# Optimization experiments

Measured on AMD Instinct MI355X. Metric: run time of the kernel, lower is better.

The kernel has to match this reference:

```python
import jax, jax.numpy as jnp
import numpy as np

B, M, D, OUT = 16384, 4096, 512, 128


def setup_inputs() -> dict:
    key = jax.random.key(0)
    ks = jax.random.split(key, 5)
    x = jax.random.normal(ks[0], (B, D), dtype=jnp.float32)
    support = jax.random.normal(ks[1], (M, D), dtype=jnp.float32)
    gamma = jnp.float32(1.0)
    head_w = jax.random.normal(ks[2], (OUT, M), dtype=jnp.float32) / np.sqrt(M)
    head_b = jax.random.normal(ks[3], (OUT,), dtype=jnp.float32) * 0.01
    scale = jnp.ones((1,), dtype=jnp.float32)
    shift = jnp.zeros((1,), dtype=jnp.float32)
    return {"x": x, "support": support, "gamma": gamma,
            "head_w": head_w, "head_b": head_b,
            "scale": scale, "shift": shift}


def reference(x, support, gamma, head_w, head_b, scale, shift):
    x2 = jnp.sum(x * x, axis=-1, keepdims=True)           # [B, 1]
    s2 = jnp.sum(support * support, axis=-1)              # [M]
    xs = jnp.einsum('bd,md->bm', x, support)              # [B, M]
    sqdist = jnp.maximum(x2 + s2[None, :] - 2.0 * xs, 0.0)
    k = jnp.exp(-gamma * sqdist)                          # RBF kernel [B, M]
    out = jnp.einsum('bm,om->bo', k, head_w) + head_b     # linear head [B, OUT]
    return scale * out + shift
```

## Files before the change

kernel.cpp:

```cpp
#include <hip/hip_runtime.h>

typedef unsigned int u32;
typedef unsigned short u16;
typedef unsigned char u8;
typedef __attribute__((ext_vector_type(8))) __bf16 bf16x8;
typedef __attribute__((ext_vector_type(4))) float f32x4;

#define NB 16384
#define NM 4096
#define ND 512
#define NOUT 128
#define L2E 1.44269504088896340736f


#define WAITLG(N) do { asm volatile("s_waitcnt vmcnt(" #N ") lgkmcnt(0)" ::: "memory"); \
                       __builtin_amdgcn_sched_barrier(0); } while (0)
#define SB0() __builtin_amdgcn_sched_barrier(0)

__device__ __forceinline__ u16 f2bf(float f) {
  u32 u = __float_as_uint(f);
  u += 0x7FFFu + ((u >> 16) & 1u);
  return (u16)(u >> 16);
}

__device__ __forceinline__ u8 f2fp8(float f) {
  u32 u = __float_as_uint(f);
  u32 s = (u >> 24) & 0x80u;
  u32 au = u & 0x7FFFFFFFu;
  if (au < 0x3C800000u) return (u8)s;
  au += 0x000FFFFFu + ((au >> 20) & 1u);
  u32 e = (au >> 23) - 120u;
  u32 m = (au >> 20) & 7u;
  return (u8)(s | (e << 3) | m);
}

__device__ __forceinline__ void stage16(const void* g, void* l) {
  __builtin_amdgcn_global_load_lds((__attribute__((address_space(1))) void*)g,
                                   (__attribute__((address_space(3))) void*)l,
                                   16, 0, 0);
}

__device__ __forceinline__ uint4 pack8bf(float4 v0, float4 v1) {
  uint4 pk;
  pk.x = (u32)f2bf(v0.x) | ((u32)f2bf(v0.y) << 16);
  pk.y = (u32)f2bf(v0.z) | ((u32)f2bf(v0.w) << 16);
  pk.z = (u32)f2bf(v1.x) | ((u32)f2bf(v1.y) << 16);
  pk.w = (u32)f2bf(v1.z) | ((u32)f2bf(v1.w) << 16);
  return pk;
}

__device__ __forceinline__ uint2 pack8f8(float4 v0, float4 v1) {
  uint2 pk;
  pk.x = (u32)f2fp8(v0.x) | ((u32)f2fp8(v0.y) << 8) |
         ((u32)f2fp8(v0.z) << 16) | ((u32)f2fp8(v0.w) << 24);
  pk.y = (u32)f2fp8(v1.x) | ((u32)f2fp8(v1.y) << 8) |
         ((u32)f2fp8(v1.z) << 16) | ((u32)f2fp8(v1.w) << 24);
  return pk;
}

__global__ __launch_bounds__(256) void prep_all(const float* __restrict__ x,
                                                const float* __restrict__ s,
                                                const float* __restrict__ hw,
                                                const float* __restrict__ gamma_p,
                                                u8*  __restrict__ x_ws,
                                                u8*  __restrict__ s_ws,
                                                u16* __restrict__ hw_ws,
                                                float* __restrict__ x2g,
                                                float* __restrict__ s2g,
                                                float* __restrict__ out) {
  __shared__ uint2 t8[2048];
  __shared__ uint4 t16[2048];
  const int tid = threadIdx.x, bid = blockIdx.x;
  const int lane = tid & 63, w = tid >> 6;

  if (bid < 640) {
    const bool isx = bid < 512;
    const int blk = isx ? bid : (bid - 512);
    const float* src_m = isx ? x : s;
    u8*    dst_ws = isx ? x_ws : s_ws;
    float* sq_out = isx ? x2g : s2g;
    const float gl   = gamma_p[0] * L2E;
    const float cmul = isx ? 1.0f : (-2.0f * gl);
    const int big  = isx ? (blk >> 1) : (blk >> 2);
    const int roff = isx ? ((blk & 1) * 32) : ((blk & 3) * 32);
    const int rows = isx ? 64 : 128;

    #pragma unroll
    for (int p = 0; p < 8; ++p) {
      const int row = p * 4 + w;
      const float* src = src_m + (size_t)(blk * 32 + row) * ND + lane * 8;
      float4 v0 = *(const float4*)src;
      float4 v1 = *(const float4*)(src + 4);
      float ss = v0.x*v0.x + v0.y*v0.y + v0.z*v0.z + v0.w*v0.w
               + v1.x*v1.x + v1.y*v1.y + v1.z*v1.z + v1.w*v1.w;
      #pragma unroll
      for (int off = 32; off > 0; off >>= 1) ss += __shfl_down(ss, off);
      if (lane == 0) sq_out[blk * 32 + row] = gl * ss;
      v0.x *= cmul; v0.y *= cmul; v0.z *= cmul; v0.w *= cmul;
      v1.x *= cmul; v1.y *= cmul; v1.z *= cmul; v1.w *= cmul;
      t8[lane * 32 + ((row + lane) & 31)] = pack8f8(v0, v1);
    }
    __syncthreads();
    #pragma unroll
    for (int p = 0; p < 8; ++p) {
      const int kg = p * 8 + (tid >> 5);
      const int row = tid & 31;
      uint2 pk = t8[kg * 32 + ((row + kg) & 31)];
      *(uint2*)&dst_ws[(((size_t)(big * 64 + kg)) * rows + roff + row) * 8] = pk;
    }
  } else if (bid < 672) {
    const int blk = bid - 640;
    #pragma unroll
    for (int p = 0; p < 8; ++p) {
      const int o = p * 16 + (tid >> 4);
      const int kg = tid & 15;
      const float* src = hw + (size_t)o * NM + blk * 128 + kg * 8;
      float4 v0 = *(const float4*)src;
      float4 v1 = *(const float4*)(src + 4);
      t16[o * 16 + ((kg + o) & 15)] = pack8bf(v0, v1);
    }
    __syncthreads();
    #pragma unroll
    for (int it = 0; it < 8; ++it) {
      const int kg = it * 2 + (tid >> 7);
      const int o = tid & 127;
      uint4 pk = t16[o * 16 + ((kg + o) & 15)];
      *(uint4*)&hw_ws[(((size_t)(blk * 16 + kg)) * 128 + o) * 8] = pk;
    }
  } else {
    float4* o4 = (float4*)out;
    const float4 z = {0.f, 0.f, 0.f, 0.f};
    size_t base = (size_t)(bid - 672) * 8192 + tid;
    #pragma unroll 8
    for (int i = 0; i < 32; ++i) o4[base + (size_t)i * 256] = z;
  }
}

__global__ __launch_bounds__(256, 2)
void rbf_fused(const u8* __restrict__ x_ws, const u8* __restrict__ s_ws,
               const u16* __restrict__ hw_ws, const float* __restrict__ x2g,
               const float* __restrict__ s2g, const float* __restrict__ head_b,
               const float* __restrict__ scale_p, const float* __restrict__ shift_p,
               float* __restrict__ out)
{
  extern __shared__ __align__(16) char smem[];

  const int tid  = threadIdx.x;
  const int w    = tid >> 6;
  const int lane = tid & 63;
  const int quad = lane >> 4;
  const int l16  = lane & 15;
  const int wr   = w & 1;
  const int wc   = w >> 1;
  const int xcd  = blockIdx.x & 7;
  const int rb   = (blockIdx.x >> 3) * 2 + (xcd & 1);
  const int half = xcd >> 1;
  const int b0   = rb * 64;

  const float vscale = scale_p[0];
  const float vshift = shift_p[0];

  const u8* xsrc = x_ws + (size_t)rb * 32768;
  const u8* ssrc = s_ws + (size_t)(half * 8) * 65536;

  auto stage_grp = [&](int mt_s, int grp_s) {
    const u8* sp = ssrc + (size_t)mt_s * 65536 + grp_s * 8192;
    char* dp = smem + 32768 + (grp_s & 3) * 8192;
    stage16(sp + tid * 16, dp + tid * 16);
    stage16(sp + 4096 + tid * 16, dp + 4096 + tid * 16);
  };

  #pragma unroll
  for (int i = 0; i < 8; ++i)
    stage16(xsrc + i * 4096 + tid * 16, smem + i * 4096 + tid * 16);
  SB0();

  f32x4 x2v[2];
  #pragma unroll
  for (int r = 0; r < 2; ++r)
    x2v[r] = *(const f32x4*)&x2g[b0 + wr * 32 + r * 16 + quad * 4];

  stage_grp(0, 0); SB0();
  stage_grp(0, 1); SB0();
  stage_grp(0, 2);
  asm volatile("s_waitcnt vmcnt(4)" ::: "memory");
  SB0();
  __builtin_amdgcn_s_barrier();
  SB0();

  const f32x4 zf = {0.f, 0.f, 0.f, 0.f};
  f32x4 acc_xs[2][4];
  f32x4 acc_out[2][4];
  #pragma unroll
  for (int r = 0; r < 2; ++r)
    #pragma unroll
    for (int c = 0; c < 4; ++c) { acc_xs[r][c] = zf; acc_out[r][c] = zf; }

  bf16x8 b2a[4], b2b[4];

  #pragma unroll 1
  for (int mt = 0; mt < 8; ++mt) {
    const int mtg = half * 8 + mt;
    float s2v[4];

    #pragma unroll
    for (int grp = 0; grp < 8; ++grp) {
      if (grp == 0) {
        #pragma unroll
        for (int c = 0; c < 4; ++c)
          s2v[c] = s2g[mtg * 128 + wc * 64 + c * 16 + l16];
      }

      long long a[2][2], b[2][4];
      #pragma unroll
      for (int k2 = 0; k2 < 2; ++k2) {
        const int kc = grp * 2 + k2;
        #pragma unroll
        for (int r = 0; r < 2; ++r)
          a[k2][r] = *(const long long*)(smem + ((kc * 4 + quad) * 64 + wr * 32 + r * 16 + l16) * 8);
        #pragma unroll
        for (int c = 0; c < 4; ++c)
          b[k2][c] = *(const long long*)(smem + 32768 + (grp & 3) * 8192 +
                                         ((k2 * 4 + quad) * 128 + wc * 64 + c * 16 + l16) * 8);
      }

      bf16x8 a2[2];
      if (mt > 0 && (grp & 1) == 0) {
        const int kg = (grp >> 1) * 4 + quad;
        #pragma unroll
        for (int r = 0; r < 2; ++r)
          a2[r] = *(const bf16x8*)(smem + 65536 + (kg * 64 + wr * 32 + r * 16 + l16) * 16);
      }

      if ((grp & 1) == 0 && !(mt == 7 && grp == 6)) {
        const int gc = (grp + 2) & 7;
        const int mc = mt + (grp == 6);
        int slab_mt = half * 8 + mc - 1; if (slab_mt < 0) slab_mt = 0;
        const int kgc = (gc >> 1) * 4 + quad;
        const size_t sb = (size_t)(slab_mt * 16 + kgc);
        #pragma unroll
        for (int c = 0; c < 4; ++c) {
          bf16x8 v = *(const bf16x8*)(hw_ws + (sb * 128 + wc * 64 + c * 16 + l16) * 8);
          if (((grp >> 1) & 1) == 0) b2a[c] = v; else b2b[c] = v;
        }
      }

      SB0();

      if (grp <= 4)      stage_grp(mt, grp + 3);
      else if (mt < 7)   stage_grp(mt + 1, grp - 5);

      if (grp == 0 || grp == 1)  WAITLG(12);
      else if (grp <= 4)         WAITLG(8);
      else if (grp == 5)         { if (mt < 7) WAITLG(8); else WAITLG(6); }
      else                       { if (mt < 7) WAITLG(8); else WAITLG(0); }

      __builtin_amdgcn_s_barrier();
      SB0();

      __builtin_amdgcn_s_setprio(1);
      #pragma unroll
      for (int k2 = 0; k2 < 2; ++k2)
        #pragma unroll
        for (int r = 0; r < 2; ++r)
          #pragma unroll
          for (int c = 0; c < 4; ++c)
            acc_xs[r][c] = __builtin_amdgcn_mfma_f32_16x16x32_fp8_fp8(a[k2][r], b[k2][c],
                                                                      acc_xs[r][c], 0, 0, 0);
      if (mt > 0 && (grp & 1) == 0) {
        #pragma unroll
        for (int r = 0; r < 2; ++r)
          #pragma unroll
          for (int c = 0; c < 4; ++c) {
            bf16x8 bb = ((((grp >> 1) + 1) & 1) == 0) ? b2a[c] : b2b[c];
            acc_out[r][c] = __builtin_amdgcn_mfma_f32_16x16x32_bf16(a2[r], bb,
                                                                    acc_out[r][c], 0, 0, 0);
          }
      }
      __builtin_amdgcn_s_setprio(0);
    }

    {
      #pragma unroll
      for (int r = 0; r < 2; ++r)
        #pragma unroll
        for (int c = 0; c < 4; ++c) {
          const int cl = wc * 64 + c * 16 + l16;
          char* kbase = smem + 65536 + (cl >> 3) * 1024 + (cl & 7) * 2;
          #pragma unroll
          for (int i = 0; i < 4; ++i) {
            const int row = wr * 32 + r * 16 + quad * 4 + i;
            const float t = acc_xs[r][c][i] + x2v[r][i] + s2v[c];
            float kv = __builtin_amdgcn_exp2f(-t);
            kv = fminf(kv, 1.0f);
            *(u16*)(kbase + row * 16) = (u16)(__float_as_uint(kv) >> 16);
            acc_xs[r][c][i] = 0.0f;
          }
        }
    }
    asm volatile("s_waitcnt lgkmcnt(0)" ::: "memory");
    SB0();
    __builtin_amdgcn_s_barrier();
    SB0();
  }

  #pragma unroll
  for (int ks = 0; ks < 4; ++ks) {
    const int kg = ks * 4 + quad;
    const size_t slab = (size_t)((half * 8 + 7) * 16 + kg);
    bf16x8 b2[4], a2[2];
    #pragma unroll
    for (int c = 0; c < 4; ++c)
      b2[c] = *(const bf16x8*)(hw_ws + (slab * 128 + wc * 64 + c * 16 + l16) * 8);
    #pragma unroll
    for (int r = 0; r < 2; ++r)
      a2[r] = *(const bf16x8*)(smem + 65536 + (kg * 64 + wr * 32 + r * 16 + l16) * 16);
    #pragma unroll
    for (int r = 0; r < 2; ++r)
      #pragma unroll
      for (int c = 0; c < 4; ++c)
        acc_out[r][c] = __builtin_amdgcn_mfma_f32_16x16x32_bf16(a2[r], b2[c], acc_out[r][c], 0, 0, 0);
  }

  float addv[4];
  #pragma unroll
  for (int c = 0; c < 4; ++c) {
    const int col = wc * 64 + c * 16 + l16;
    addv[c] = (half == 0) ? (vscale * head_b[col] + vshift) : 0.0f;
  }
  #pragma unroll
  for (int r = 0; r < 2; ++r)
    #pragma unroll
    for (int c = 0; c < 4; ++c) {
      const int col = wc * 64 + c * 16 + l16;
      #pragma unroll
      for (int i = 0; i < 4; ++i) {
        const int row = b0 + wr * 32 + r * 16 + quad * 4 + i;
        atomicAdd(&out[(size_t)row * NOUT + col], vscale * acc_out[r][c][i] + addv[c]);
      }
    }
}

extern "C" void kernel_launch(void* const* d_in, const int* in_sizes, int n_in,
                              void* d_out, int out_size, void* d_ws, size_t ws_size,
                              hipStream_t stream) {
  const float* x       = (const float*)d_in[0];
  const float* support = (const float*)d_in[1];
  const float* gamma   = (const float*)d_in[2];
  const float* head_w  = (const float*)d_in[3];
  const float* head_b  = (const float*)d_in[4];
  const float* scale   = (const float*)d_in[5];
  const float* shift   = (const float*)d_in[6];
  float* out = (float*)d_out;

  char* w = (char*)d_ws;
  u8*    x_ws  = (u8*)(w);
  u8*    s_ws  = (u8*)(w + 8388608);
  u16*   hw_ws = (u16*)(w + 10485760);
  float* x2g   = (float*)(w + 11534336);
  float* s2g   = (float*)(w + 11599872);

  static bool lds_init = false;
  if (!lds_init) {
    hipFuncSetAttribute(reinterpret_cast<const void*>(rbf_fused),
                        hipFuncAttributeMaxDynamicSharedMemorySize, 81920);
    lds_init = true;
  }

  prep_all<<<736, 256, 0, stream>>>(x, support, head_w, gamma,
                                    x_ws, s_ws, hw_ws, x2g, s2g, out);
  rbf_fused<<<1024, 256, 81920, stream>>>(x_ws, s_ws, hw_ws, x2g, s2g,
                                          head_b, scale, shift, out);
}
```

Baseline: 176.2 us.

## Use 512-thread blocks with register-resident x tile and smaller LDS

Doubles the block to 8 waves, each owning a 16-row slice instead of 32 rows, and keeps the x fp8 operand in registers rather than staging it through LDS. Shared memory shrinks from 80KB dynamic to 48KB static, which is meant to allow more waves per CU and better latency hiding. Head-weight prefetch now uses inline asm global loads with a single buffer, and the vmcnt waits are retuned. The cost is more register pressure per wave (16 preloaded x fragments), a tighter waitcnt schedule, and more redundant hw loads across waves.

```diff
diff --git a/kernel.cpp b/kernel.cpp
--- a/kernel.cpp
+++ b/kernel.cpp
@@ -5,6 +5,7 @@
 typedef unsigned char u8;
 typedef __attribute__((ext_vector_type(8))) __bf16 bf16x8;
 typedef __attribute__((ext_vector_type(4))) float f32x4;
+typedef __attribute__((ext_vector_type(4))) int i32x4;
 
 #define NB 16384
 #define NM 4096
@@ -38,6 +39,12 @@
   __builtin_amdgcn_global_load_lds((__attribute__((address_space(1))) void*)g,
                                    (__attribute__((address_space(3))) void*)l,
                                    16, 0, 0);
+}
+
+__device__ __forceinline__ bf16x8 ldg_b128(const void* p) {
+  i32x4 r;
+  asm volatile("global_load_dwordx4 %0, %1, off" : "=&v"(r) : "v"(p) : "memory");
+  return __builtin_bit_cast(bf16x8, r);
 }
 
 __device__ __forceinline__ uint4 pack8bf(float4 v0, float4 v1) {
@@ -136,22 +143,22 @@
   }
 }
 
-__global__ __launch_bounds__(256, 2)
+__global__ __launch_bounds__(512, 4)
 void rbf_fused(const u8* __restrict__ x_ws, const u8* __restrict__ s_ws,
                const u16* __restrict__ hw_ws, const float* __restrict__ x2g,
                const float* __restrict__ s2g, const float* __restrict__ head_b,
                const float* __restrict__ scale_p, const float* __restrict__ shift_p,
                float* __restrict__ out)
 {
-  extern __shared__ __align__(16) char smem[];
+  __shared__ __align__(16) char smem[49152];
 
   const int tid  = threadIdx.x;
   const int w    = tid >> 6;
   const int lane = tid & 63;
   const int quad = lane >> 4;
   const int l16  = lane & 15;
-  const int wr   = w & 1;
-  const int wc   = w >> 1;
+  const int wr   = w & 3;
+  const int wc   = w >> 2;
   const int xcd  = blockIdx.x & 7;
   const int rb   = (blockIdx.x >> 3) * 2 + (xcd & 1);
   const int half = xcd >> 1;
@@ -163,40 +170,31 @@
   const u8* xsrc = x_ws + (size_t)rb * 32768;
   const u8* ssrc = s_ws + (size_t)(half * 8) * 65536;
 
-  auto stage_grp = [&](int mt_s, int grp_s) {
+  auto stage_grp = [&](int mt_s, int grp_s, int buf) {
     const u8* sp = ssrc + (size_t)mt_s * 65536 + grp_s * 8192;
-    char* dp = smem + 32768 + (grp_s & 3) * 8192;
-    stage16(sp + tid * 16, dp + tid * 16);
-    stage16(sp + 4096 + tid * 16, dp + 4096 + tid * 16);
+    stage16(sp + tid * 16, smem + buf * 8192 + tid * 16);
   };
 
-  #pragma unroll
-  for (int i = 0; i < 8; ++i)
-    stage16(xsrc + i * 4096 + tid * 16, smem + i * 4096 + tid * 16);
+  long long xr[16];
+  #pragma unroll
+  for (int kc = 0; kc < 16; ++kc)
+    xr[kc] = *(const long long*)(xsrc + ((kc * 4 + quad) * 64 + wr * 16 + l16) * 8);
+  f32x4 x2v = *(const f32x4*)&x2g[b0 + wr * 16 + quad * 4];
   SB0();
-
-  f32x4 x2v[2];
-  #pragma unroll
-  for (int r = 0; r < 2; ++r)
-    x2v[r] = *(const f32x4*)&x2g[b0 + wr * 32 + r * 16 + quad * 4];
-
-  stage_grp(0, 0); SB0();
-  stage_grp(0, 1); SB0();
-  stage_grp(0, 2);
-  asm volatile("s_waitcnt vmcnt(4)" ::: "memory");
+  stage_grp(0, 0, 0); SB0();
+  stage_grp(0, 1, 1); SB0();
+  stage_grp(0, 2, 2);
+  asm volatile("s_waitcnt vmcnt(2)" ::: "memory");
   SB0();
   __builtin_amdgcn_s_barrier();
   SB0();
 
   const f32x4 zf = {0.f, 0.f, 0.f, 0.f};
-  f32x4 acc_xs[2][4];
-  f32x4 acc_out[2][4];
-  #pragma unroll
-  for (int r = 0; r < 2; ++r)
-    #pragma unroll
-    for (int c = 0; c < 4; ++c) { acc_xs[r][c] = zf; acc_out[r][c] = zf; }
-
-  bf16x8 b2a[4], b2b[4];
+  f32x4 acc_xs[4], acc_out[4];
+  #pragma unroll
+  for (int c = 0; c < 4; ++c) { acc_xs[c] = zf; acc_out[c] = zf; }
+
+  bf16x8 b2[4];
 
   #pragma unroll 1
   for (int mt = 0; mt < 8; ++mt) {
@@ -205,55 +203,45 @@
 
     #pragma unroll
     for (int grp = 0; grp < 8; ++grp) {
-      if (grp == 0) {
-        #pragma unroll
-        for (int c = 0; c < 4; ++c)
-          s2v[c] = s2g[mtg * 128 + wc * 64 + c * 16 + l16];
-      }
-
-      long long a[2][2], b[2][4];
+      long long bf[2][4];
       #pragma unroll
-      for (int k2 = 0; k2 < 2; ++k2) {
-        const int kc = grp * 2 + k2;
-        #pragma unroll
-        for (int r = 0; r < 2; ++r)
-          a[k2][r] = *(const long long*)(smem + ((kc * 4 + quad) * 64 + wr * 32 + r * 16 + l16) * 8);
-        #pragma unroll
-        for (int c = 0; c < 4; ++c)
-          b[k2][c] = *(const long long*)(smem + 32768 + (grp & 3) * 8192 +
-                                         ((k2 * 4 + quad) * 128 + wc * 64 + c * 16 + l16) * 8);
-      }
-
-      bf16x8 a2[2];
+      for (int k2 = 0; k2 < 2; ++k2)
+        #pragma unroll
+        for (int c = 0; c < 4; ++c)
+          bf[k2][c] = *(const long long*)(smem + (grp & 3) * 8192 +
+                                          ((k2 * 4 + quad) * 128 + wc * 64 + c * 16 + l16) * 8);
+      bf16x8 a2;
       if (mt > 0 && (grp & 1) == 0) {
         const int kg = (grp >> 1) * 4 + quad;
-        #pragma unroll
-        for (int r = 0; r < 2; ++r)
-          a2[r] = *(const bf16x8*)(smem + 65536 + (kg * 64 + wr * 32 + r * 16 + l16) * 16);
-      }
-
-      if ((grp & 1) == 0 && !(mt == 7 && grp == 6)) {
-        const int gc = (grp + 2) & 7;
-        const int mc = mt + (grp == 6);
-        int slab_mt = half * 8 + mc - 1; if (slab_mt < 0) slab_mt = 0;
-        const int kgc = (gc >> 1) * 4 + quad;
-        const size_t sb = (size_t)(slab_mt * 16 + kgc);
-        #pragma unroll
-        for (int c = 0; c < 4; ++c) {
-          bf16x8 v = *(const bf16x8*)(hw_ws + (sb * 128 + wc * 64 + c * 16 + l16) * 8);
-          if (((grp >> 1) & 1) == 0) b2a[c] = v; else b2b[c] = v;
-        }
+        a2 = *(const bf16x8*)(smem + 32768 + kg * 1024 + (wr * 16 + l16) * 16);
+      }
+      if (grp == 0) {
+        #pragma unroll
+        for (int c = 0; c < 4; ++c)
+          s2v[c] = s2g[mtg * 128 + wc * 64 + c * 16 + l16];
+      }
+      if ((grp & 1) == 1 && !(mt == 7 && grp == 7)) {
+        int ks, sm;
+        if (grp < 7) { ks = (grp + 1) >> 1; sm = mtg - 1; }
+        else         { ks = 0;              sm = mtg;     }
+        if (sm < 0) sm = 0;
+        const int kg = ks * 4 + quad;
+        const size_t sb = (size_t)(sm * 16 + kg);
+        #pragma unroll
+        for (int c = 0; c < 4; ++c)
+          b2[c] = ldg_b128(hw_ws + (sb * 128 + wc * 64 + c * 16 + l16) * 8);
       }
 
       SB0();
 
-      if (grp <= 4)      stage_grp(mt, grp + 3);
-      else if (mt < 7)   stage_grp(mt + 1, grp - 5);
-
-      if (grp == 0 || grp == 1)  WAITLG(12);
-      else if (grp <= 4)         WAITLG(8);
-      else if (grp == 5)         { if (mt < 7) WAITLG(8); else WAITLG(6); }
-      else                       { if (mt < 7) WAITLG(8); else WAITLG(0); }
+      if (grp <= 4)     stage_grp(mt, grp + 3, (grp + 3) & 3);
+      else if (mt < 7)  stage_grp(mt + 1, grp - 5, (grp + 3) & 3);
+
+      if (grp == 2 || grp == 4)  WAITLG(2);
+      else if (grp == 6)         { if (mt < 7) WAITLG(2); else WAITLG(0); }
+      else if (grp == 5)         { if (mt < 7) WAITLG(6); else WAITLG(5); }
+      else if (grp == 7)         { if (mt < 7) WAITLG(6); else WAITLG(0); }
+      else                       WAITLG(6);
 
       __builtin_amdgcn_s_barrier();
       SB0();
@@ -262,41 +250,30 @@
       #pragma unroll
       for (int k2 = 0; k2 < 2; ++k2)
         #pragma unroll
-        for (int r = 0; r < 2; ++r)
-          #pragma unroll
-          for (int c = 0; c < 4; ++c)
-            acc_xs[r][c] = __builtin_amdgcn_mfma_f32_16x16x32_fp8_fp8(a[k2][r], b[k2][c],
-                                                                      acc_xs[r][c], 0, 0, 0);
+        for (int c = 0; c < 4; ++c)
+          acc_xs[c] = __builtin_amdgcn_mfma_f32_16x16x32_fp8_fp8(xr[grp * 2 + k2], bf[k2][c],
+                                                                 acc_xs[c], 0, 0, 0);
       if (mt > 0 && (grp & 1) == 0) {
         #pragma unroll
-        for (int r = 0; r < 2; ++r)
-          #pragma unroll
-          for (int c = 0; c < 4; ++c) {
-            bf16x8 bb = ((((grp >> 1) + 1) & 1) == 0) ? b2a[c] : b2b[c];
-            acc_out[r][c] = __builtin_amdgcn_mfma_f32_16x16x32_bf16(a2[r], bb,
-                                                                    acc_out[r][c], 0, 0, 0);
-          }
+        for (int c = 0; c < 4; ++c)
+          acc_out[c] = __builtin_amdgcn_mfma_f32_16x16x32_bf16(a2, b2[c], acc_out[c], 0, 0, 0);
       }
       __builtin_amdgcn_s_setprio(0);
     }
 
-    {
+    #pragma unroll
+    for (int c = 0; c < 4; ++c) {
+      const int cl = wc * 64 + c * 16 + l16;
+      char* kbase = smem + 32768 + (cl >> 3) * 1024 + (cl & 7) * 2;
       #pragma unroll
-      for (int r = 0; r < 2; ++r)
-        #pragma unroll
-        for (int c = 0; c < 4; ++c) {
-          const int cl = wc * 64 + c * 16 + l16;
-          char* kbase = smem + 65536 + (cl >> 3) * 1024 + (cl & 7) * 2;
-          #pragma unroll
-          for (int i = 0; i < 4; ++i) {
-            const int row = wr * 32 + r * 16 + quad * 4 + i;
-            const float t = acc_xs[r][c][i] + x2v[r][i] + s2v[c];
-            float kv = __builtin_amdgcn_exp2f(-t);
-            kv = fminf(kv, 1.0f);
-            *(u16*)(kbase + row * 16) = (u16)(__float_as_uint(kv) >> 16);
-            acc_xs[r][c][i] = 0.0f;
-          }
-        }
+      for (int i = 0; i < 4; ++i) {
+        const int row = wr * 16 + quad * 4 + i;
+        const float t = acc_xs[c][i] + x2v[i] + s2v[c];
+        float kv = __builtin_amdgcn_exp2f(-t);
+        kv = fminf(kv, 1.0f);
+        *(u16*)(kbase + row * 16) = (u16)(__float_as_uint(kv) >> 16);
+        acc_xs[c][i] = 0.0f;
+      }
     }
     asm volatile("s_waitcnt lgkmcnt(0)" ::: "memory");
     SB0();
@@ -307,19 +284,15 @@
   #pragma unroll
   for (int ks = 0; ks < 4; ++ks) {
     const int kg = ks * 4 + quad;
-    const size_t slab = (size_t)((half * 8 + 7) * 16 + kg);
-    bf16x8 b2[4], a2[2];
+    const size_t sb = (size_t)((half * 8 + 7) * 16 + kg);
+    bf16x8 bb[4];
     #pragma unroll
     for (int c = 0; c < 4; ++c)
-      b2[c] = *(const bf16x8*)(hw_ws + (slab * 128 + wc * 64 + c * 16 + l16) * 8);
-    #pragma unroll
-    for (int r = 0; r < 2; ++r)
-      a2[r] = *(const bf16x8*)(smem + 65536 + (kg * 64 + wr * 32 + r * 16 + l16) * 16);
-    #pragma unroll
-    for (int r = 0; r < 2; ++r)
-      #pragma unroll
-      for (int c = 0; c < 4; ++c)
-        acc_out[r][c] = __builtin_amdgcn_mfma_f32_16x16x32_bf16(a2[r], b2[c], acc_out[r][c], 0, 0, 0);
+      bb[c] = *(const bf16x8*)(hw_ws + (sb * 128 + wc * 64 + c * 16 + l16) * 8);
+    bf16x8 a2 = *(const bf16x8*)(smem + 32768 + kg * 1024 + (wr * 16 + l16) * 16);
+    #pragma unroll
+    for (int c = 0; c < 4; ++c)
+      acc_out[c] = __builtin_amdgcn_mfma_f32_16x16x32_bf16(a2, bb[c], acc_out[c], 0, 0, 0);
   }
 
   float addv[4];
@@ -329,16 +302,14 @@
     addv[c] = (half == 0) ? (vscale * head_b[col] + vshift) : 0.0f;
   }
   #pragma unroll
-  for (int r = 0; r < 2; ++r)
-    #pragma unroll
-    for (int c = 0; c < 4; ++c) {
-      const int col = wc * 64 + c * 16 + l16;
-      #pragma unroll
-      for (int i = 0; i < 4; ++i) {
-        const int row = b0 + wr * 32 + r * 16 + quad * 4 + i;
-        atomicAdd(&out[(size_t)row * NOUT + col], vscale * acc_out[r][c][i] + addv[c]);
-      }
-    }
+  for (int c = 0; c < 4; ++c) {
+    const int col = wc * 64 + c * 16 + l16;
+    #pragma unroll
+    for (int i = 0; i < 4; ++i) {
+      const int row = b0 + wr * 16 + quad * 4 + i;
+      atomicAdd(&out[(size_t)row * NOUT + col], vscale * acc_out[c][i] + addv[c]);
+    }
+  }
 }
 
 extern "C" void kernel_launch(void* const* d_in, const int* in_sizes, int n_in,
@@ -360,15 +331,8 @@
   float* x2g   = (float*)(w + 11534336);
   float* s2g   = (float*)(w + 11599872);
 
-  static bool lds_init = false;
-  if (!lds_init) {
-    hipFuncSetAttribute(reinterpret_cast<const void*>(rbf_fused),
-                        hipFuncAttributeMaxDynamicSharedMemorySize, 81920);
-    lds_init = true;
-  }
-
   prep_all<<<736, 256, 0, stream>>>(x, support, head_w, gamma,
                                     x_ws, s_ws, hw_ws, x2g, s2g, out);
-  rbf_fused<<<1024, 256, 81920, stream>>>(x_ws, s_ws, hw_ws, x2g, s2g,
-                                          head_b, scale, shift, out);
-}
+  rbf_fused<<<1024, 512, 0, stream>>>(x_ws, s_ws, hw_ws, x2g, s2g,
+                                      head_b, scale, shift, out);
+}
```

After: 225.8 us. 28.1% more time.

## Double-buffer LDS fragment reads and interleave them with FP8 MFMA groups

Applied to the files above, without the earlier changes.

Restructures the fused distance/RBF/head kernel's inner loop so the FP8 A/B fragments for the next k-group are read from LDS into a ping-pong register buffer between the two MFMA halves of the current group. The head-weight global loads now go through inline asm, and the bf16 kernel-tile reads are hoisted to the start of each M tile. The goal is to hide LDS latency behind MFMA issue and to simplify the waitcnt schedule. In exchange it raises register pressure (extra fragment and a2h buffers), and the hand-tuned vmcnt counts must match the new load order exactly.

```diff
diff --git a/kernel.cpp b/kernel.cpp
--- a/kernel.cpp
+++ b/kernel.cpp
@@ -5,6 +5,7 @@
 typedef unsigned char u8;
 typedef __attribute__((ext_vector_type(8))) __bf16 bf16x8;
 typedef __attribute__((ext_vector_type(4))) float f32x4;
+typedef __attribute__((ext_vector_type(4))) int i32x4;
 
 #define NB 16384
 #define NM 4096
@@ -38,6 +39,12 @@
   __builtin_amdgcn_global_load_lds((__attribute__((address_space(1))) void*)g,
                                    (__attribute__((address_space(3))) void*)l,
                                    16, 0, 0);
+}
+
+__device__ __forceinline__ bf16x8 ldg_b128(const void* p) {
+  i32x4 r;
+  asm volatile("global_load_dwordx4 %0, %1, off" : "=&v"(r) : "v"(p) : "memory");
+  return __builtin_bit_cast(bf16x8, r);
 }
 
 __device__ __forceinline__ uint4 pack8bf(float4 v0, float4 v1) {
@@ -170,24 +177,41 @@
     stage16(sp + 4096 + tid * 16, dp + 4096 + tid * 16);
   };
 
+  f32x4 x2v[2];
+  #pragma unroll
+  for (int r = 0; r < 2; ++r)
+    x2v[r] = *(const f32x4*)&x2g[b0 + wr * 32 + r * 16 + quad * 4];
+  SB0();
   #pragma unroll
   for (int i = 0; i < 8; ++i)
     stage16(xsrc + i * 4096 + tid * 16, smem + i * 4096 + tid * 16);
   SB0();
-
-  f32x4 x2v[2];
-  #pragma unroll
-  for (int r = 0; r < 2; ++r)
-    x2v[r] = *(const f32x4*)&x2g[b0 + wr * 32 + r * 16 + quad * 4];
-
   stage_grp(0, 0); SB0();
   stage_grp(0, 1); SB0();
   stage_grp(0, 2);
-  asm volatile("s_waitcnt vmcnt(4)" ::: "memory");
+  asm volatile("s_waitcnt vmcnt(2)" ::: "memory");
   SB0();
   __builtin_amdgcn_s_barrier();
   SB0();
 
+  long long aF[2][2][2];
+  long long bF[2][2][4];
+  bf16x8 b2[2][4];
+  bf16x8 a2h[4][2];
+
+  #pragma unroll
+  for (int k2 = 0; k2 < 2; ++k2) {
+    #pragma unroll
+    for (int r = 0; r < 2; ++r)
+      aF[0][k2][r] = *(const long long*)(smem + ((k2 * 4 + quad) * 64 + wr * 32 + r * 16 + l16) * 8);
+    #pragma unroll
+    for (int c = 0; c < 4; ++c)
+      bF[0][k2][c] = *(const long long*)(smem + 32768 +
+                       ((k2 * 4 + quad) * 128 + wc * 64 + c * 16 + l16) * 8);
+  }
+  asm volatile("s_waitcnt lgkmcnt(0)" ::: "memory");
+  SB0();
+
   const f32x4 zf = {0.f, 0.f, 0.f, 0.f};
   f32x4 acc_xs[2][4];
   f32x4 acc_out[2][4];
@@ -196,88 +220,105 @@
     #pragma unroll
     for (int c = 0; c < 4; ++c) { acc_xs[r][c] = zf; acc_out[r][c] = zf; }
 
-  bf16x8 b2a[4], b2b[4];
-
   #pragma unroll 1
   for (int mt = 0; mt < 8; ++mt) {
     const int mtg = half * 8 + mt;
+
+    if (mt > 0) {
+      #pragma unroll
+      for (int ks = 0; ks < 4; ++ks) {
+        const int kg = ks * 4 + quad;
+        #pragma unroll
+        for (int r = 0; r < 2; ++r)
+          a2h[ks][r] = *(const bf16x8*)(smem + 65536 + (kg * 64 + wr * 32 + r * 16 + l16) * 16);
+      }
+      asm volatile("s_waitcnt lgkmcnt(0)" ::: "memory");
+      SB0();
+    }
     float s2v[4];
+    #pragma unroll
+    for (int c = 0; c < 4; ++c)
+      s2v[c] = s2g[mtg * 128 + wc * 64 + c * 16 + l16];
+    SB0();
 
     #pragma unroll
     for (int grp = 0; grp < 8; ++grp) {
-      if (grp == 0) {
+      const int p  = grp & 1;
+      const int pn = p ^ 1;
+      const int gN = grp + 1;
+      const bool doRd = !(mt == 7 && grp == 7);
+
+      __builtin_amdgcn_s_setprio(1);
+      #pragma unroll
+      for (int r = 0; r < 2; ++r)
         #pragma unroll
         for (int c = 0; c < 4; ++c)
-          s2v[c] = s2g[mtg * 128 + wc * 64 + c * 16 + l16];
-      }
-
-      long long a[2][2], b[2][4];
-      #pragma unroll
-      for (int k2 = 0; k2 < 2; ++k2) {
-        const int kc = grp * 2 + k2;
-        #pragma unroll
-        for (int r = 0; r < 2; ++r)
-          a[k2][r] = *(const long long*)(smem + ((kc * 4 + quad) * 64 + wr * 32 + r * 16 + l16) * 8);
+          acc_xs[r][c] = __builtin_amdgcn_mfma_f32_16x16x32_fp8_fp8(
+              aF[p][0][r], bF[p][0][c], acc_xs[r][c], 0, 0, 0);
+      __builtin_amdgcn_s_setprio(0);
+      SB0();
+      if (doRd) {
+        #pragma unroll
+        for (int k2 = 0; k2 < 2; ++k2)
+          #pragma unroll
+          for (int r = 0; r < 2; ++r)
+            aF[pn][k2][r] = *(const long long*)(smem +
+                ((((gN & 7) * 2 + k2) * 4 + quad) * 64 + wr * 32 + r * 16 + l16) * 8);
+        #pragma unroll
+        for (int c = 0; c < 2; ++c)
+          bF[pn][0][c] = *(const long long*)(smem + 32768 + (gN & 3) * 8192 +
+              ((0 * 4 + quad) * 128 + wc * 64 + c * 16 + l16) * 8);
+      }
+      SB0();
+      __builtin_amdgcn_s_setprio(1);
+      #pragma unroll
+      for (int r = 0; r < 2; ++r)
         #pragma unroll
         for (int c = 0; c < 4; ++c)
-          b[k2][c] = *(const long long*)(smem + 32768 + (grp & 3) * 8192 +
-                                         ((k2 * 4 + quad) * 128 + wc * 64 + c * 16 + l16) * 8);
-      }
-
-      bf16x8 a2[2];
+          acc_xs[r][c] = __builtin_amdgcn_mfma_f32_16x16x32_fp8_fp8(
+              aF[p][1][r], bF[p][1][c], acc_xs[r][c], 0, 0, 0);
+      __builtin_amdgcn_s_setprio(0);
+      SB0();
+      if (doRd) {
+        #pragma unroll
+        for (int c = 2; c < 4; ++c)
+          bF[pn][0][c] = *(const long long*)(smem + 32768 + (gN & 3) * 8192 +
+              ((0 * 4 + quad) * 128 + wc * 64 + c * 16 + l16) * 8);
+        #pragma unroll
+        for (int c = 0; c < 4; ++c)
+          bF[pn][1][c] = *(const long long*)(smem + 32768 + (gN & 3) * 8192 +
+              ((1 * 4 + quad) * 128 + wc * 64 + c * 16 + l16) * 8);
+      }
+      SB0();
       if (mt > 0 && (grp & 1) == 0) {
-        const int kg = (grp >> 1) * 4 + quad;
-        #pragma unroll
-        for (int r = 0; r < 2; ++r)
-          a2[r] = *(const bf16x8*)(smem + 65536 + (kg * 64 + wr * 32 + r * 16 + l16) * 16);
-      }
-
-      if ((grp & 1) == 0 && !(mt == 7 && grp == 6)) {
-        const int gc = (grp + 2) & 7;
-        const int mc = mt + (grp == 6);
-        int slab_mt = half * 8 + mc - 1; if (slab_mt < 0) slab_mt = 0;
-        const int kgc = (gc >> 1) * 4 + quad;
-        const size_t sb = (size_t)(slab_mt * 16 + kgc);
-        #pragma unroll
-        for (int c = 0; c < 4; ++c) {
-          bf16x8 v = *(const bf16x8*)(hw_ws + (sb * 128 + wc * 64 + c * 16 + l16) * 8);
-          if (((grp >> 1) & 1) == 0) b2a[c] = v; else b2b[c] = v;
-        }
-      }
-
-      SB0();
-
-      if (grp <= 4)      stage_grp(mt, grp + 3);
-      else if (mt < 7)   stage_grp(mt + 1, grp - 5);
-
-      if (grp == 0 || grp == 1)  WAITLG(12);
-      else if (grp <= 4)         WAITLG(8);
-      else if (grp == 5)         { if (mt < 7) WAITLG(8); else WAITLG(6); }
-      else                       { if (mt < 7) WAITLG(8); else WAITLG(0); }
-
-      __builtin_amdgcn_s_barrier();
-      SB0();
-
-      __builtin_amdgcn_s_setprio(1);
-      #pragma unroll
-      for (int k2 = 0; k2 < 2; ++k2)
+        __builtin_amdgcn_s_setprio(1);
         #pragma unroll
         for (int r = 0; r < 2; ++r)
           #pragma unroll
           for (int c = 0; c < 4; ++c)
-            acc_xs[r][c] = __builtin_amdgcn_mfma_f32_16x16x32_fp8_fp8(a[k2][r], b[k2][c],
-                                                                      acc_xs[r][c], 0, 0, 0);
-      if (mt > 0 && (grp & 1) == 0) {
-        #pragma unroll
-        for (int r = 0; r < 2; ++r)
-          #pragma unroll
-          for (int c = 0; c < 4; ++c) {
-            bf16x8 bb = ((((grp >> 1) + 1) & 1) == 0) ? b2a[c] : b2b[c];
-            acc_out[r][c] = __builtin_amdgcn_mfma_f32_16x16x32_bf16(a2[r], bb,
-                                                                    acc_out[r][c], 0, 0, 0);
-          }
-      }
-      __builtin_amdgcn_s_setprio(0);
+            acc_out[r][c] = __builtin_amdgcn_mfma_f32_16x16x32_bf16(
+                a2h[grp >> 1][r], b2[(grp >> 1) & 1][c], acc_out[r][c], 0, 0, 0);
+        __builtin_amdgcn_s_setprio(0);
+      }
+      SB0();
+      if (grp <= 4)     stage_grp(mt, grp + 3);
+      else if (mt < 7)  stage_grp(mt + 1, grp - 5);
+      if ((grp & 1) == 0 && !(mt == 7 && grp == 6)) {
+        const int gs = (grp + 2) & 7;
+        const int ms = mt + (grp == 6);
+        int sl = half * 8 + ms - 1; if (sl < 0) sl = 0;
+        const int kg = (gs >> 1) * 4 + quad;
+        const size_t sb = (size_t)(sl * 16 + kg);
+        #pragma unroll
+        for (int c = 0; c < 4; ++c)
+          b2[((grp >> 1) + 1) & 1][c] = ldg_b128(hw_ws + (sb * 128 + wc * 64 + c * 16 + l16) * 8);
+      }
+
+      if (mt == 7 && grp >= 5)   WAITLG(0);
+      else if ((grp & 1) == 0)   WAITLG(6);
+      else                       WAITLG(2);
+      __builtin_amdgcn_s_barrier();
+      SB0();
     }
 
     {
@@ -307,11 +348,11 @@
   #pragma unroll
   for (int ks = 0; ks < 4; ++ks) {
     const int kg = ks * 4 + quad;
-    const size_t slab = (size_t)((half * 8 + 7) * 16 + kg);
-    bf16x8 b2[4], a2[2];
+    const size_t sb = (size_t)((half * 8 + 7) * 16 + kg);
+    bf16x8 bb[4], a2[2];
     #pragma unroll
     for (int c = 0; c < 4; ++c)
-      b2[c] = *(const bf16x8*)(hw_ws + (slab * 128 + wc * 64 + c * 16 + l16) * 8);
+      bb[c] = *(const bf16x8*)(hw_ws + (sb * 128 + wc * 64 + c * 16 + l16) * 8);
     #pragma unroll
     for (int r = 0; r < 2; ++r)
       a2[r] = *(const bf16x8*)(smem + 65536 + (kg * 64 + wr * 32 + r * 16 + l16) * 16);
@@ -319,7 +360,7 @@
     for (int r = 0; r < 2; ++r)
       #pragma unroll
       for (int c = 0; c < 4; ++c)
-        acc_out[r][c] = __builtin_amdgcn_mfma_f32_16x16x32_bf16(a2[r], b2[c], acc_out[r][c], 0, 0, 0);
+        acc_out[r][c] = __builtin_amdgcn_mfma_f32_16x16x32_bf16(a2[r], bb[c], acc_out[r][c], 0, 0, 0);
   }
 
   float addv[4];
```

After: 182.3 us. 3.4% more time.
